# Performance work log

Hardware: AMD Instinct MI355X
Metric: run time of the kernel (lower is better)

Reference implementation:

```python
import jax, jax.numpy as jnp
import numpy as np


def setup_inputs() -> dict:
    key = jax.random.key(0)
    k1, k2 = jax.random.split(key)
    feature = jax.random.normal(k1, (4, 256, 60, 60), dtype=jnp.float32)
    mask_q = jax.random.uniform(k2, (4, 2, 60, 60), dtype=jnp.float32)
    return {"feature": feature, "mask_q": mask_q, "kernel": 1}


FG_THRES = 0.5
BG_THRES = 0.8
TOPK_FALLBACK = 12


def _sel_mask(p, thres):
    # boolean selection mask; falls back to top-12 pixels if nothing passes threshold
    m = p > thres
    topk_idx = jax.lax.top_k(p, TOPK_FALLBACK)[1]
    topk_m = jnp.zeros(p.shape, bool).at[topk_idx].set(True)
    return jnp.where(m.sum() > 0, m, topk_m)


def _ssp_single(feat, pred):
    # feat: [C, N], pred: [2, N] (ch0 = bg, ch1 = fg)
    pred_bg, pred_fg = pred[0], pred[1]
    fg_m = _sel_mask(pred_fg, FG_THRES)
    bg_m = _sel_mask(pred_bg, BG_THRES)

    def proto(m):
        mf = m.astype(feat.dtype)
        return (feat * mf[None, :]).sum(-1) / mf.sum()  # mean over selected cols

    fg_proto = proto(fg_m)  # [C]
    bg_proto = proto(bg_m)  # [C]

    # column-normalized features; selected-column sub-matmul == full matmul with
    # column-masked softmax (masked logits -> zero weight), identical math
    featn = feat / jnp.linalg.norm(feat, axis=0, keepdims=True)
    sim = (featn.T @ featn) * 2.0  # [N, N]
    logits = jnp.where(bg_m[None, :], sim, jnp.finfo(sim.dtype).min)
    w = jax.nn.softmax(logits, axis=-1)  # weights zero outside bg selection
    bg_local = (w @ feat.T).T  # [C, N]; == bg_sim @ bg_feat.T in torch code
    return fg_proto, bg_proto, bg_local


def reference(feature, mask_q, kernel):
    # kernel=True path of SSP_MatchingNet.forward: returns (FP_1, BP_1)
    bs, C, fh, fw = feature.shape
    feat_flat = feature.reshape(bs, C, fh * fw)
    pred = mask_q.reshape(bs, 2, -1)
    fg_p, bg_p, bg_loc = jax.vmap(_ssp_single)(feat_flat, pred)
    FP_1 = fg_p[:, :, None, None] * 1.0  # SSFP_1
    BP_1 = bg_p[:, :, None, None] * 0.3 + bg_loc.reshape(bs, C, fh, fw) * 0.7
    return FP_1, BP_1
```

## Files before the change

kernel.cpp:

```cpp
#include <hip/hip_runtime.h>
#include <math.h>
#include <float.h>

#define NPix 3600
#define NC   256
#define NB   4
#define MCAP 768

typedef __attribute__((ext_vector_type(8))) _Float16 half8v;
typedef __attribute__((ext_vector_type(4))) float float4v;

__device__ __forceinline__ unsigned short f2h(float x) {
  _Float16 h = (_Float16)x;
  unsigned short u; __builtin_memcpy(&u, &h, 2); return u;
}
__device__ __forceinline__ float h2f(unsigned short u) {
  _Float16 h; __builtin_memcpy(&h, &u, 2); return (float)h;
}

__device__ __forceinline__ void gld_lds16(const void* g, void* l) {
  __builtin_amdgcn_global_load_lds(
      (const __attribute__((address_space(1))) unsigned int*)g,
      (__attribute__((address_space(3))) unsigned int*)l, 16, 0, 0);
}

__global__ __launch_bounds__(256) void k_colnorm(const float* __restrict__ feature,
                                                 float* __restrict__ colnorm) {
  int b = blockIdx.y;
  int n = blockIdx.x * 256 + threadIdx.x;
  if (n >= NPix) return;
  const float* feat = feature + (size_t)b * NC * NPix;
  float acc = 0.f;
#pragma unroll 8
  for (int c = 0; c < NC; ++c) {
    float v = feat[(size_t)c * NPix + n];
    acc += v * v;
  }
  colnorm[b * NPix + n] = sqrtf(acc);
}

__device__ void block_top12(const float* __restrict__ p, int t,
                            float* s_rv, int* s_ri, int* s_chosen) {
  for (int k = 0; k < 12; ++k) {
    float best = -FLT_MAX;
    int bi = 0x7fffffff;
    for (int n = t; n < NPix; n += 1024) {
      bool excl = false;
      for (int j = 0; j < k; ++j)
        if (s_chosen[j] == n) excl = true;
      if (!excl) {
        float v = p[n];
        if (v > best || (v == best && n < bi)) { best = v; bi = n; }
      }
    }
    s_rv[t] = best; s_ri[t] = bi;
    __syncthreads();
    for (int d = 512; d > 0; d >>= 1) {
      if (t < d) {
        if (s_rv[t + d] > s_rv[t] ||
            (s_rv[t + d] == s_rv[t] && s_ri[t + d] < s_ri[t])) {
          s_rv[t] = s_rv[t + d]; s_ri[t] = s_ri[t + d];
        }
      }
      __syncthreads();
    }
    if (t == 0) s_chosen[k] = s_ri[0];
    __syncthreads();
  }
  if (t == 0) {
    for (int a = 1; a < 12; ++a) {
      int key = s_chosen[a]; int j = a - 1;
      while (j >= 0 && s_chosen[j] > key) { s_chosen[j + 1] = s_chosen[j]; --j; }
      s_chosen[j + 1] = key;
    }
  }
  __syncthreads();
}

__global__ __launch_bounds__(1024) void k_mask(const float* __restrict__ mask_q,
                                               unsigned char* __restrict__ fgm,
                                               unsigned char* __restrict__ bgm,
                                               int* __restrict__ bgsel,
                                               int* __restrict__ cnts) {
  int b = blockIdx.x;
  int t = threadIdx.x;
  int wv = t >> 6, l = t & 63;
  const float* pred_bg = mask_q + (size_t)b * 2 * NPix;
  const float* pred_fg = pred_bg + NPix;

  __shared__ int   s_wtot[16];
  __shared__ int   s_base[2];
  __shared__ float s_rv[1024];
  __shared__ int   s_ri[1024];
  __shared__ int   s_chosen[12];

  if (t == 0) { s_base[0] = 0; s_base[1] = 0; }
  __syncthreads();

  unsigned long long lmask = (1ull << l) - 1ull;

  for (int chunk = 0; chunk < NPix; chunk += 1024) {
    int n = chunk + t;
    int fgf = 0, bgf = 0;
    if (n < NPix) {
      fgf = pred_fg[n] > 0.5f ? 1 : 0;
      bgf = pred_bg[n] > 0.8f ? 1 : 0;
      fgm[b * NPix + n] = (unsigned char)fgf;
      bgm[b * NPix + n] = (unsigned char)bgf;
    }
    unsigned long long fb = __ballot(fgf != 0);
    unsigned long long bb = __ballot(bgf != 0);
    if (l == 0) s_wtot[wv] = __popcll(fb) | (__popcll(bb) << 16);
    __syncthreads();
    int fsum = 0, bsum = 0, bpre = 0;
#pragma unroll
    for (int w = 0; w < 16; ++w) {
      int v = s_wtot[w];
      if (w < wv) bpre += (v >> 16);
      fsum += v & 0xffff; bsum += (v >> 16);
    }
    if (bgf) {
      int pos = s_base[1] + bpre + (int)__popcll(bb & lmask);
      bgsel[b * NPix + pos] = n;
    }
    __syncthreads();
    if (t == 0) { s_base[0] += fsum; s_base[1] += bsum; }
    __syncthreads();
  }
  int fgcnt = s_base[0];
  int bgcnt = s_base[1];

  if (fgcnt == 0) {
    block_top12(pred_fg, t, s_rv, s_ri, s_chosen);
    if (t < 12) fgm[b * NPix + s_chosen[t]] = 1;
    fgcnt = 12;
    __syncthreads();
  }
  if (bgcnt == 0) {
    block_top12(pred_bg, t, s_rv, s_ri, s_chosen);
    if (t < 12) {
      bgm[b * NPix + s_chosen[t]] = 1;
      bgsel[b * NPix + t] = s_chosen[t];
    }
    bgcnt = 12;
    __syncthreads();
  }
  if (t == 0) { cnts[b] = fgcnt; cnts[4 + b] = bgcnt; }
}

__global__ __launch_bounds__(256) void k_proto(const float* __restrict__ feature,
                                               const unsigned char* __restrict__ fgm,
                                               const unsigned char* __restrict__ bgm,
                                               const int* __restrict__ cnts,
                                               float* __restrict__ out,
                                               float* __restrict__ bgproto) {
  int c = blockIdx.x, b = blockIdx.y, t = threadIdx.x;
  const float* frow = feature + ((size_t)b * NC + c) * NPix;
  float fs = 0.f, bs = 0.f;
  for (int n = t; n < NPix; n += 256) {
    float v = frow[n];
    fs += v * (float)fgm[b * NPix + n];
    bs += v * (float)bgm[b * NPix + n];
  }
  __shared__ float s1[256], s2[256];
  s1[t] = fs; s2[t] = bs;
  __syncthreads();
  for (int d = 128; d > 0; d >>= 1) {
    if (t < d) { s1[t] += s1[t + d]; s2[t] += s2[t + d]; }
    __syncthreads();
  }
  if (t == 0) {
    out[b * NC + c]     = s1[0] / (float)cnts[b];
    bgproto[b * NC + c] = s2[0] / (float)cnts[4 + b];
  }
}

__global__ __launch_bounds__(256) void k_normpack(const float* __restrict__ feature,
                                                  const unsigned char* __restrict__ fgm,
                                                  const unsigned char* __restrict__ bgm,
                                                  float* __restrict__ colnorm,
                                                  unsigned short* __restrict__ Qf,
                                                  float* __restrict__ pp) {
  int b = blockIdx.y, nt = blockIdx.x, t = threadIdx.x;
  int n0 = nt * 64;
  __shared__ float s_sq[16][68];
  __shared__ float s_inv[64];
  __shared__ float s_fg[64], s_bg[64];
  __shared__ unsigned int tl[64][65];
  __shared__ float traw[64][65];
  __shared__ float s_red[2][4][64];
  const float* fb = feature + (size_t)b * NC * NPix;

  int p4 = t & 15, cq = t >> 4;
  float sq0 = 0.f, sq1 = 0.f, sq2 = 0.f, sq3 = 0.f;
  if (n0 + 64 <= NPix) {
#pragma unroll
    for (int j = 0; j < 16; ++j) {
      const float* src = fb + (size_t)(cq * 16 + j) * NPix + n0 + p4 * 4;
      float4 v = *(const float4*)src;
      sq0 += v.x * v.x; sq1 += v.y * v.y; sq2 += v.z * v.z; sq3 += v.w * v.w;
    }
  } else {
#pragma unroll
    for (int j = 0; j < 16; ++j) {
      size_t base = (size_t)(cq * 16 + j) * NPix;
      int n = n0 + p4 * 4;
      float v0 = (n + 0 < NPix) ? fb[base + n + 0] : 0.f;
      float v1 = (n + 1 < NPix) ? fb[base + n + 1] : 0.f;
      float v2 = (n + 2 < NPix) ? fb[base + n + 2] : 0.f;
      float v3 = (n + 3 < NPix) ? fb[base + n + 3] : 0.f;
      sq0 += v0 * v0; sq1 += v1 * v1; sq2 += v2 * v2; sq3 += v3 * v3;
    }
  }
  s_sq[cq][p4 * 4 + 0] = sq0;
  s_sq[cq][p4 * 4 + 1] = sq1;
  s_sq[cq][p4 * 4 + 2] = sq2;
  s_sq[cq][p4 * 4 + 3] = sq3;
  __syncthreads();
  if (t < 64) {
    float acc = 0.f;
#pragma unroll
    for (int q = 0; q < 16; ++q) acc += s_sq[q][t];
    float nrm = sqrtf(acc);
    int n = n0 + t;
    s_inv[t] = (n < NPix) ? 1.f / nrm : 0.f;
    if (n < NPix) colnorm[b * NPix + n] = nrm;
    s_fg[t] = (n < NPix) ? (float)fgm[b * NPix + n] : 0.f;
    s_bg[t] = (n < NPix) ? (float)bgm[b * NPix + n] : 0.f;
  }
  __syncthreads();

  unsigned short* QfB = Qf + (size_t)b * NPix * NC;
  int nl = t & 63;
  int nn = n0 + nl;
  bool inr = nn < NPix;
  float invn = s_inv[nl];
  for (int cs = 0; cs < 4; ++cs) {
    int c0 = cs * 64;
#pragma unroll
    for (int i = 0; i < 16; ++i) {
      int cl = (t >> 6) + 4 * i;
      float raw = inr ? fb[(size_t)(c0 + cl) * NPix + nn] : 0.f;
      traw[cl][nl] = raw;
      tl[cl][nl] = (unsigned int)f2h(raw * invn);
    }
    __syncthreads();
#pragma unroll
    for (int i = 0; i < 8; ++i) {
      int idx = t + 256 * i;
      int n = idx >> 5;
      int cp = idx & 31;
      int row = n0 + n;
      if (row < NPix) {
        unsigned int u = (tl[2 * cp][n] & 0xffffu) | (tl[2 * cp + 1][n] << 16);
        *(unsigned int*)&QfB[(size_t)row * NC + c0 + 2 * cp] = u;
      }
    }
    {
      int cl = t & 63, pq = t >> 6;
      float pf = 0.f, pb = 0.f;
#pragma unroll
      for (int k = 0; k < 16; ++k) {
        int p = pq * 16 + k;
        float feat = traw[cl][p];
        pf += feat * s_fg[p];
        pb += feat * s_bg[p];
      }
      s_red[0][pq][cl] = pf;
      s_red[1][pq][cl] = pb;
    }
    __syncthreads();
    if (t < 128) {
      int m = t >> 6, cl = t & 63;
      float s = s_red[m][0][cl] + s_red[m][1][cl] + s_red[m][2][cl] + s_red[m][3][cl];
      pp[((size_t)(b * 57 + nt) * 2 + m) * 256 + c0 + cl] = s;
    }
    __syncthreads();
  }
}

__global__ __launch_bounds__(256) void k_vg(const unsigned short* __restrict__ Qf,
                                            const float* __restrict__ colnorm,
                                            const int* __restrict__ cnts,
                                            const int* __restrict__ bgsel,
                                            unsigned short* __restrict__ Vg,
                                            const float* __restrict__ pp,
                                            float* __restrict__ out,
                                            float* __restrict__ bgproto,
                                            unsigned short* __restrict__ wbuf,
                                            float* __restrict__ wpart) {
  int b = blockIdx.z;
  int x = blockIdx.x;
  int t = threadIdx.x;

  __shared__ __align__(16) char smem[32768];

  if (x == 222) {
    int c = t;
    float f = 0.f, g = 0.f;
    for (int nt = 0; nt < 57; ++nt) {
      const float* base = pp + (size_t)(b * 57 + nt) * 2 * 256;
      f += base[c];
      g += base[256 + c];
    }
    out[b * NC + c]     = f / (float)cnts[b];
    bgproto[b * NC + c] = g / (float)cnts[4 + b];
    return;
  }

  int M = cnts[4 + b];
  if (M > MCAP) return;

  if (x >= 174) {
    int u = x - 174;
    int jt = u >> 2, cs = u & 3;
    int j0 = jt * 64, c0 = cs * 64;
    unsigned short* tl = (unsigned short*)smem;
    const size_t qoff = (size_t)b * NPix * NC;
#pragma unroll
    for (int i = 0; i < 16; ++i) {
      int idx = t + 256 * i; int j = idx >> 6, ch = idx & 63;
      int jg = j0 + j;
      float v = 0.f;
      if (jg < M) {
        int src = bgsel[b * NPix + jg];
        v = h2f(Qf[qoff + (size_t)src * NC + c0 + ch]) * colnorm[b * NPix + src];
      }
      tl[j * 73 + ch] = f2h(v);
    }
    __syncthreads();
#pragma unroll
    for (int i = 0; i < 16; ++i) {
      int idx = t + 256 * i; int ch = idx >> 6, j = idx & 63;
      Vg[((size_t)b * NC + c0 + ch) * MCAP + j0 + j] = tl[j * 73 + ch];
    }
    return;
  }

  int rt = x % 29, jt = x / 29;
  if (jt * 128 >= M) return;
  int wv = t >> 6, l = t & 63;
  int n0 = rt * 128, j0 = jt * 128;

  unsigned short* Ah = (unsigned short*)smem;
  unsigned short* Bh = (unsigned short*)(smem + 32768 / 2);

  const unsigned short* QfB = Qf + (size_t)b * NPix * NC;

  size_t asrc[4];
  int    aslt[4];
#pragma unroll
  for (int i = 0; i < 4; ++i) {
    int u = i * 256 + wv * 64 + l;
    int r = u >> 3, sl = u & 7;
    int grow = n0 + r; if (grow > NPix - 1) grow = NPix - 1;
    asrc[i] = (size_t)grow * NC;
    aslt[i] = (sl ^ (r & 7)) << 3;
  }
  size_t bsrc[4];
  int    bslt[4];
#pragma unroll
  for (int i = 0; i < 4; ++i) {
    int u = i * 256 + wv * 64 + l;
    int r = u >> 3, sl = u & 7;
    int jg = j0 + r;
    int src = (jg < M) ? bgsel[b * NPix + jg] : 0;
    bsrc[i] = (size_t)src * NC;
    bslt[i] = (sl ^ (r & 7)) << 3;
  }

  int lr = l & 15;
  int lk = l >> 4;

  float4v acc[2][8];
#pragma unroll
  for (int rf = 0; rf < 2; ++rf)
#pragma unroll
    for (int cf = 0; cf < 8; ++cf) { float4v z = {0.f,0.f,0.f,0.f}; acc[rf][cf] = z; }

  for (int cc = 0; cc < 4; ++cc) {
    int cbase = cc * 64;
#pragma unroll
    for (int i = 0; i < 4; ++i) {
      int ldso = (i * 256 + wv * 64) * 16;
      gld_lds16(QfB + asrc[i] + cbase + aslt[i], (char*)Ah + ldso);
    }
#pragma unroll
    for (int i = 0; i < 4; ++i) {
      int ldso = (i * 256 + wv * 64) * 16;
      gld_lds16(QfB + bsrc[i] + cbase + bslt[i], (char*)Bh + ldso);
    }
    __syncthreads();

#pragma unroll
    for (int kk = 0; kk < 2; ++kk) {
      int kslot = kk * 4 + lk;
      half8v ah[2];
#pragma unroll
      for (int rf = 0; rf < 2; ++rf) {
        int r = wv * 32 + rf * 16 + lr;
        int s = (kslot ^ (r & 7)) << 3;
        ah[rf] = *(const half8v*)&Ah[r * 64 + s];
      }
#pragma unroll
      for (int cf = 0; cf < 8; ++cf) {
        int j = cf * 16 + lr;
        int s = (kslot ^ (j & 7)) << 3;
        half8v bh = *(const half8v*)&Bh[j * 64 + s];
#pragma unroll
        for (int rf = 0; rf < 2; ++rf)
          acc[rf][cf] = __builtin_amdgcn_mfma_f32_16x16x32_f16(ah[rf], bh, acc[rf][cf], 0, 0, 0);
      }
    }
    __syncthreads();
  }

  float rs[2][4];
#pragma unroll
  for (int rf = 0; rf < 2; ++rf)
#pragma unroll
    for (int i = 0; i < 4; ++i) rs[rf][i] = 0.f;

#pragma unroll
  for (int rf = 0; rf < 2; ++rf)
#pragma unroll
    for (int cf = 0; cf < 8; ++cf)
#pragma unroll
      for (int i = 0; i < 4; ++i) {
        int row = n0 + wv * 32 + rf * 16 + lk * 4 + i;
        int j = j0 + cf * 16 + lr;
        float s = acc[rf][cf][i];
        unsigned short w16 = (j < M) ? f2h(__expf(2.f * s - 2.f)) : (unsigned short)0;
        if (row < NPix)
          wbuf[((size_t)b * NPix + row) * MCAP + j] = w16;
        rs[rf][i] += h2f(w16);
      }

#pragma unroll
  for (int rf = 0; rf < 2; ++rf)
#pragma unroll
    for (int i = 0; i < 4; ++i) {
      float v = rs[rf][i];
      v += __shfl_xor(v, 1);
      v += __shfl_xor(v, 2);
      v += __shfl_xor(v, 4);
      v += __shfl_xor(v, 8);
      int row = n0 + wv * 32 + rf * 16 + lk * 4 + i;
      if (lr == 0 && row < NPix)
        wpart[((size_t)b * NPix + row) * 12 + jt] = v;
    }
}

__global__ __launch_bounds__(256, 3) void k_gemm2e(const unsigned short* __restrict__ wbuf,
                                                   const unsigned short* __restrict__ Vg,
                                                   const int* __restrict__ cnts,
                                                   const float* __restrict__ wpart,
                                                   const float* __restrict__ bgproto,
                                                   float* __restrict__ out) {
  int b = blockIdx.z; int M = cnts[4 + b]; if (M > MCAP) return;
  int rt = blockIdx.x, cs = blockIdx.y;
  int t = threadIdx.x, wv = t >> 6, l = t & 63;
  int n0 = rt * 128, c0 = cs * 128;
  int arow0 = n0 + wv * 32 + (l & 15);
  int arow1 = arow0 + 16;
  if (arow0 > NPix - 1) arow0 = NPix - 1;
  if (arow1 > NPix - 1) arow1 = NPix - 1;
  const unsigned short* wr0 = wbuf + ((size_t)b * NPix + arow0) * MCAP + (l >> 4) * 8;
  const unsigned short* wr1 = wbuf + ((size_t)b * NPix + arow1) * MCAP + (l >> 4) * 8;
  const unsigned short* vb  = Vg + ((size_t)b * NC + c0 + (l & 15)) * MCAP + (l >> 4) * 8;

  __shared__ float trans[64][129];
  __shared__ float s_linv[128];
  __shared__ float s_bp[128];

  float4v acc[2][8];
#pragma unroll
  for (int rf = 0; rf < 2; ++rf)
#pragma unroll
    for (int cf = 0; cf < 8; ++cf) { float4v z = {0.f,0.f,0.f,0.f}; acc[rf][cf] = z; }

  int nkk = (M + 31) >> 5;
  for (int kk = 0; kk < nkk; ++kk) {
    half8v a0 = *(const half8v*)(wr0 + kk * 32);
    half8v a1 = *(const half8v*)(wr1 + kk * 32);
#pragma unroll
    for (int cf = 0; cf < 8; ++cf) {
      half8v bv = *(const half8v*)(vb + (size_t)cf * 16 * MCAP + kk * 32);
      acc[0][cf] = __builtin_amdgcn_mfma_f32_16x16x32_f16(a0, bv, acc[0][cf], 0, 0, 0);
      acc[1][cf] = __builtin_amdgcn_mfma_f32_16x16x32_f16(a1, bv, acc[1][cf], 0, 0, 0);
    }
  }

  if (t < 128) {
    int row = n0 + t;
    if (row < NPix) {
      const float* wp = wpart + ((size_t)b * NPix + row) * 12;
      int njt = (M + 127) >> 7;
      float s = 0.f;
      for (int j = 0; j < njt; ++j) s += wp[j];
      s_linv[t] = 1.f / s;
    } else s_linv[t] = 0.f;
    s_bp[t] = bgproto[b * NC + c0 + t];
  }

  int g = l >> 4;
  float* outBP = out + NB * NC;
#pragma unroll
  for (int half = 0; half < 2; ++half) {
    __syncthreads();
#pragma unroll
    for (int cfl = 0; cfl < 4; ++cfl) {
      int cf = half * 4 + cfl;
#pragma unroll
      for (int rf = 0; rf < 2; ++rf)
#pragma unroll
        for (int i = 0; i < 4; ++i) {
          int c_l = cfl * 16 + (l & 15);
          int n_l = wv * 32 + rf * 16 + g * 4 + i;
          trans[c_l][n_l] = acc[rf][cf][i];
        }
    }
    __syncthreads();
#pragma unroll
    for (int it = 0; it < 8; ++it) {
      int idx = t + 256 * it;
      int c_l = idx >> 5;
      int q   = idx & 31;
      int n   = n0 + q * 4;
      if (n < NPix) {
        float bpv = s_bp[half * 64 + c_l];
        float4 o;
        o.x = bpv * 0.3f + trans[c_l][q * 4 + 0] * s_linv[q * 4 + 0] * 0.7f;
        o.y = bpv * 0.3f + trans[c_l][q * 4 + 1] * s_linv[q * 4 + 1] * 0.7f;
        o.z = bpv * 0.3f + trans[c_l][q * 4 + 2] * s_linv[q * 4 + 2] * 0.7f;
        o.w = bpv * 0.3f + trans[c_l][q * 4 + 3] * s_linv[q * 4 + 3] * 0.7f;
        *(float4*)&outBP[((size_t)b * NC + c0 + half * 64 + c_l) * NPix + n] = o;
      }
    }
  }
}

__global__ __launch_bounds__(256) void k_attn(const float* __restrict__ feature,
                                              const float* __restrict__ colnorm,
                                              const int* __restrict__ cnts,
                                              const int* __restrict__ bgsel,
                                              const float* __restrict__ bgproto,
                                              float* __restrict__ out,
                                              int gate) {
  int b = blockIdx.y;
  int M = cnts[4 + b];
  if (gate && M <= MCAP) return;
  int tile = blockIdx.x;
  int t = threadIdx.x;
  int rl  = t >> 4;
  int l16 = t & 15;
  int row = tile * 16 + rl;
  const float* feat = feature + (size_t)b * NC * NPix;

  __shared__ float s_k[32][NC];
  __shared__ float s_vn[32];

  float inv_n = 1.f / colnorm[b * NPix + row];
  float q[16];
#pragma unroll
  for (int k = 0; k < 4; ++k)
#pragma unroll
    for (int i = 0; i < 4; ++i) {
      int c = l16 * 4 + 64 * k + i;
      q[k * 4 + i] = feat[(size_t)c * NPix + row] * inv_n;
    }

  float l_acc = 0.f;
  float O[16];
#pragma unroll
  for (int i = 0; i < 16; ++i) O[i] = 0.f;

  for (int kt = 0; kt < M; kt += 32) {
    int jmax = min(32, M - kt);
    __syncthreads();
    for (int u = t; u < 32 * 64; u += 256) {
      int jj = u >> 6;
      int cc = (u & 63) << 2;
      if (jj < jmax) {
        int src = bgsel[b * NPix + kt + jj];
        float inv = 1.f / colnorm[b * NPix + src];
        float4 v;
        v.x = feat[(size_t)(cc + 0) * NPix + src] * inv;
        v.y = feat[(size_t)(cc + 1) * NPix + src] * inv;
        v.z = feat[(size_t)(cc + 2) * NPix + src] * inv;
        v.w = feat[(size_t)(cc + 3) * NPix + src] * inv;
        *(float4*)&s_k[jj][cc] = v;
      }
    }
    if (t < 32)
      s_vn[t] = (t < jmax) ? colnorm[b * NPix + bgsel[b * NPix + kt + t]] : 0.f;
    __syncthreads();

    for (int j = 0; j < jmax; ++j) {
      float kv[16];
      float s = 0.f;
#pragma unroll
      for (int k = 0; k < 4; ++k) {
        float4 v4 = *(const float4*)&s_k[j][l16 * 4 + 64 * k];
        kv[k * 4 + 0] = v4.x; kv[k * 4 + 1] = v4.y;
        kv[k * 4 + 2] = v4.z; kv[k * 4 + 3] = v4.w;
        s += q[k * 4 + 0] * v4.x + q[k * 4 + 1] * v4.y +
             q[k * 4 + 2] * v4.z + q[k * 4 + 3] * v4.w;
      }
      s += __shfl_xor(s, 1);
      s += __shfl_xor(s, 2);
      s += __shfl_xor(s, 4);
      s += __shfl_xor(s, 8);
      float e = __expf(2.f * s - 2.f);
      l_acc += e;
      float ev = e * s_vn[j];
#pragma unroll
      for (int i = 0; i < 16; ++i) O[i] += ev * kv[i];
    }
  }

  float inv_l = 1.f / l_acc;
  float* outBP = out + NB * NC;
  const float* bp = bgproto + b * NC;
#pragma unroll
  for (int k = 0; k < 4; ++k)
#pragma unroll
    for (int i = 0; i < 4; ++i) {
      int c = l16 * 4 + 64 * k + i;
      outBP[((size_t)b * NC + c) * NPix + row] =
          bp[c] * 0.3f + O[k * 4 + i] * inv_l * 0.7f;
    }
}

extern "C" void kernel_launch(void* const* d_in, const int* in_sizes, int n_in,
                              void* d_out, int out_size, void* d_ws, size_t ws_size,
                              hipStream_t stream) {
  const float* feature = (const float*)d_in[0];
  const float* mask_q  = (const float*)d_in[1];
  float* out = (float*)d_out;
  char* ws = (char*)d_ws;

  const size_t BIG_NEED = 32428160ULL;
  if (ws_size >= BIG_NEED) {
    float* colnorm   = (float*)(ws + 0);
    float* bgproto   = (float*)(ws + 115200);
    int*   cnts      = (int*)  (ws + 119296);
    int*   bgsel     = (int*)  (ws + 119552);
    unsigned char* fgm = (unsigned char*)(ws + 177152);
    unsigned char* bgm = (unsigned char*)(ws + 191552);
    float* pp        = (float*)(ws + 205952);
    unsigned short* Vg  = (unsigned short*)(ws + 672896);
    unsigned short* Qf  = (unsigned short*)(ws + 2245760);
    unsigned short* wbuf = (unsigned short*)(ws + 9618560);
    float* wpart     = (float*)(ws + 31736960);

    k_mask    <<<NB,               1024, 0, stream>>>(mask_q, fgm, bgm, bgsel, cnts);
    k_normpack<<<dim3(57, NB),     256, 0, stream>>>(feature, fgm, bgm, colnorm, Qf, pp);
    k_vg      <<<dim3(223, 1, NB), 256, 0, stream>>>(Qf, colnorm, cnts, bgsel, Vg,
                                                     pp, out, bgproto, wbuf, wpart);
    k_gemm2e  <<<dim3(29, 2, NB),  256, 0, stream>>>(wbuf, Vg, cnts, wpart, bgproto, out);
    k_attn    <<<dim3(225, NB),    256, 0, stream>>>(feature, colnorm, cnts, bgsel,
                                                     bgproto, out, 1);
  } else {
    float* colnorm  = (float*)(ws + 0);
    float* bgproto  = (float*)(ws + 115200);
    int*   cnts     = (int*)  (ws + 119296);
    int*   bgsel    = (int*)  (ws + 119552);
    unsigned char* fgm = (unsigned char*)(ws + 177152);
    unsigned char* bgm = (unsigned char*)(ws + 191552);

    k_colnorm<<<dim3(15, NB), 256, 0, stream>>>(feature, colnorm);
    k_mask   <<<NB,           1024, 0, stream>>>(mask_q, fgm, bgm, bgsel, cnts);
    k_proto  <<<dim3(NC, NB), 256, 0, stream>>>(feature, fgm, bgm, cnts, out, bgproto);
    k_attn   <<<dim3(225, NB),256, 0, stream>>>(feature, colnorm, cnts, bgsel,
                                                bgproto, out, 0);
  }
}
```

Baseline: 91.00 us.

## Fuse fallback attention into gemm2e launch and reuse register-held features in normpack

The fallback attention path (for batches with more than MCAP selected background pixels) moves into extra blocks of the k_gemm2e launch, which removes a separate k_attn launch that mostly exited early. k_normpack now keeps the float4 feature values from its norm pass in registers and writes them into the shared transpose tiles, instead of loading the feature tensor from global memory a second time. The cost is more registers per thread in normpack (16 float4) and a larger fused kernel whose shared-memory use is the maximum of both paths. This may lower occupancy.

```diff
diff --git a/kernel.cpp b/kernel.cpp
--- a/kernel.cpp
+++ b/kernel.cpp
@@ -192,12 +192,13 @@
   const float* fb = feature + (size_t)b * NC * NPix;
 
   int p4 = t & 15, cq = t >> 4;
+  float4 raw[16];
   float sq0 = 0.f, sq1 = 0.f, sq2 = 0.f, sq3 = 0.f;
   if (n0 + 64 <= NPix) {
 #pragma unroll
     for (int j = 0; j < 16; ++j) {
-      const float* src = fb + (size_t)(cq * 16 + j) * NPix + n0 + p4 * 4;
-      float4 v = *(const float4*)src;
+      float4 v = *(const float4*)(fb + (size_t)(cq * 16 + j) * NPix + n0 + p4 * 4);
+      raw[j] = v;
       sq0 += v.x * v.x; sq1 += v.y * v.y; sq2 += v.z * v.z; sq3 += v.w * v.w;
     }
   } else {
@@ -205,11 +206,13 @@
     for (int j = 0; j < 16; ++j) {
       size_t base = (size_t)(cq * 16 + j) * NPix;
       int n = n0 + p4 * 4;
-      float v0 = (n + 0 < NPix) ? fb[base + n + 0] : 0.f;
-      float v1 = (n + 1 < NPix) ? fb[base + n + 1] : 0.f;
-      float v2 = (n + 2 < NPix) ? fb[base + n + 2] : 0.f;
-      float v3 = (n + 3 < NPix) ? fb[base + n + 3] : 0.f;
-      sq0 += v0 * v0; sq1 += v1 * v1; sq2 += v2 * v2; sq3 += v3 * v3;
+      float4 v;
+      v.x = (n + 0 < NPix) ? fb[base + n + 0] : 0.f;
+      v.y = (n + 1 < NPix) ? fb[base + n + 1] : 0.f;
+      v.z = (n + 2 < NPix) ? fb[base + n + 2] : 0.f;
+      v.w = (n + 3 < NPix) ? fb[base + n + 3] : 0.f;
+      raw[j] = v;
+      sq0 += v.x * v.x; sq1 += v.y * v.y; sq2 += v.z * v.z; sq3 += v.w * v.w;
     }
   }
   s_sq[cq][p4 * 4 + 0] = sq0;
@@ -231,18 +234,22 @@
   __syncthreads();
 
   unsigned short* QfB = Qf + (size_t)b * NPix * NC;
-  int nl = t & 63;
-  int nn = n0 + nl;
-  bool inr = nn < NPix;
-  float invn = s_inv[nl];
+  int clbase = (cq & 3) * 16;
+  int nlb = p4 * 4;
+  float inv0 = s_inv[nlb + 0], inv1 = s_inv[nlb + 1];
+  float inv2 = s_inv[nlb + 2], inv3 = s_inv[nlb + 3];
   for (int cs = 0; cs < 4; ++cs) {
     int c0 = cs * 64;
-#pragma unroll
-    for (int i = 0; i < 16; ++i) {
-      int cl = (t >> 6) + 4 * i;
-      float raw = inr ? fb[(size_t)(c0 + cl) * NPix + nn] : 0.f;
-      traw[cl][nl] = raw;
-      tl[cl][nl] = (unsigned int)f2h(raw * invn);
+    if ((cq >> 2) == cs) {
+#pragma unroll
+      for (int j = 0; j < 16; ++j) {
+        int cl = clbase + j;
+        float4 v = raw[j];
+        traw[cl][nlb + 0] = v.x;  tl[cl][nlb + 0] = (unsigned int)f2h(v.x * inv0);
+        traw[cl][nlb + 1] = v.y;  tl[cl][nlb + 1] = (unsigned int)f2h(v.y * inv1);
+        traw[cl][nlb + 2] = v.z;  tl[cl][nlb + 2] = (unsigned int)f2h(v.z * inv2);
+        traw[cl][nlb + 3] = v.w;  tl[cl][nlb + 3] = (unsigned int)f2h(v.w * inv3);
+      }
     }
     __syncthreads();
 #pragma unroll
@@ -343,7 +350,7 @@
   int n0 = rt * 128, j0 = jt * 128;
 
   unsigned short* Ah = (unsigned short*)smem;
-  unsigned short* Bh = (unsigned short*)(smem + 32768 / 2);
+  unsigned short* Bh = (unsigned short*)(smem + 16384);
 
   const unsigned short* QfB = Qf + (size_t)b * NPix * NC;
 
@@ -456,10 +463,102 @@
                                                    const int* __restrict__ cnts,
                                                    const float* __restrict__ wpart,
                                                    const float* __restrict__ bgproto,
+                                                   const float* __restrict__ feature,
+                                                   const float* __restrict__ colnorm,
+                                                   const int* __restrict__ bgsel,
                                                    float* __restrict__ out) {
-  int b = blockIdx.z; int M = cnts[4 + b]; if (M > MCAP) return;
-  int rt = blockIdx.x, cs = blockIdx.y;
-  int t = threadIdx.x, wv = t >> 6, l = t & 63;
+  int b = blockIdx.z; int M = cnts[4 + b];
+  int x = blockIdx.x;
+  int t = threadIdx.x;
+
+  __shared__ __align__(16) char smem[34816];
+
+  if (x >= 58) {
+    if (M <= MCAP) return;
+    int tile = x - 58;
+    int rl  = t >> 4;
+    int l16 = t & 15;
+    int row = tile * 16 + rl;
+    const float* feat = feature + (size_t)b * NC * NPix;
+    float* s_k  = (float*)smem;
+    float* s_vn = (float*)(smem + 32768);
+
+    float inv_n = 1.f / colnorm[b * NPix + row];
+    float q[16];
+#pragma unroll
+    for (int k = 0; k < 4; ++k)
+#pragma unroll
+      for (int i = 0; i < 4; ++i) {
+        int c = l16 * 4 + 64 * k + i;
+        q[k * 4 + i] = feat[(size_t)c * NPix + row] * inv_n;
+      }
+
+    float l_acc = 0.f;
+    float O[16];
+#pragma unroll
+    for (int i = 0; i < 16; ++i) O[i] = 0.f;
+
+    for (int kt = 0; kt < M; kt += 32) {
+      int jmax = min(32, M - kt);
+      __syncthreads();
+      for (int u = t; u < 32 * 64; u += 256) {
+        int jj = u >> 6;
+        int cc = (u & 63) << 2;
+        if (jj < jmax) {
+          int src = bgsel[b * NPix + kt + jj];
+          float inv = 1.f / colnorm[b * NPix + src];
+          float4 v;
+          v.x = feat[(size_t)(cc + 0) * NPix + src] * inv;
+          v.y = feat[(size_t)(cc + 1) * NPix + src] * inv;
+          v.z = feat[(size_t)(cc + 2) * NPix + src] * inv;
+          v.w = feat[(size_t)(cc + 3) * NPix + src] * inv;
+          *(float4*)&s_k[jj * 256 + cc] = v;
+        }
+      }
+      if (t < 32)
+        s_vn[t] = (t < jmax) ? colnorm[b * NPix + bgsel[b * NPix + kt + t]] : 0.f;
+      __syncthreads();
+
+      for (int j = 0; j < jmax; ++j) {
+        float kv[16];
+        float s = 0.f;
+#pragma unroll
+        for (int k = 0; k < 4; ++k) {
+          float4 v4 = *(const float4*)&s_k[j * 256 + l16 * 4 + 64 * k];
+          kv[k * 4 + 0] = v4.x; kv[k * 4 + 1] = v4.y;
+          kv[k * 4 + 2] = v4.z; kv[k * 4 + 3] = v4.w;
+          s += q[k * 4 + 0] * v4.x + q[k * 4 + 1] * v4.y +
+               q[k * 4 + 2] * v4.z + q[k * 4 + 3] * v4.w;
+        }
+        s += __shfl_xor(s, 1);
+        s += __shfl_xor(s, 2);
+        s += __shfl_xor(s, 4);
+        s += __shfl_xor(s, 8);
+        float e = __expf(2.f * s - 2.f);
+        l_acc += e;
+        float ev = e * s_vn[j];
+#pragma unroll
+        for (int i = 0; i < 16; ++i) O[i] += ev * kv[i];
+      }
+    }
+
+    float inv_l = 1.f / l_acc;
+    float* outBP = out + NB * NC;
+    const float* bp = bgproto + b * NC;
+#pragma unroll
+    for (int k = 0; k < 4; ++k)
+#pragma unroll
+      for (int i = 0; i < 4; ++i) {
+        int c = l16 * 4 + 64 * k + i;
+        outBP[((size_t)b * NC + c) * NPix + row] =
+            bp[c] * 0.3f + O[k * 4 + i] * inv_l * 0.7f;
+      }
+    return;
+  }
+
+  if (M > MCAP) return;
+  int rt = x % 29, cs = x / 29;
+  int wv = t >> 6, l = t & 63;
   int n0 = rt * 128, c0 = cs * 128;
   int arow0 = n0 + wv * 32 + (l & 15);
   int arow1 = arow0 + 16;
@@ -469,9 +568,9 @@
   const unsigned short* wr1 = wbuf + ((size_t)b * NPix + arow1) * MCAP + (l >> 4) * 8;
   const unsigned short* vb  = Vg + ((size_t)b * NC + c0 + (l & 15)) * MCAP + (l >> 4) * 8;
 
-  __shared__ float trans[64][129];
-  __shared__ float s_linv[128];
-  __shared__ float s_bp[128];
+  float* trans  = (float*)smem;
+  float* s_linv = (float*)(smem + 33024);
+  float* s_bp   = (float*)(smem + 33536);
 
   float4v acc[2][8];
 #pragma unroll
@@ -517,7 +616,7 @@
         for (int i = 0; i < 4; ++i) {
           int c_l = cfl * 16 + (l & 15);
           int n_l = wv * 32 + rf * 16 + g * 4 + i;
-          trans[c_l][n_l] = acc[rf][cf][i];
+          trans[c_l * 129 + n_l] = acc[rf][cf][i];
         }
     }
     __syncthreads();
@@ -530,10 +629,10 @@
       if (n < NPix) {
         float bpv = s_bp[half * 64 + c_l];
         float4 o;
-        o.x = bpv * 0.3f + trans[c_l][q * 4 + 0] * s_linv[q * 4 + 0] * 0.7f;
-        o.y = bpv * 0.3f + trans[c_l][q * 4 + 1] * s_linv[q * 4 + 1] * 0.7f;
-        o.z = bpv * 0.3f + trans[c_l][q * 4 + 2] * s_linv[q * 4 + 2] * 0.7f;
-        o.w = bpv * 0.3f + trans[c_l][q * 4 + 3] * s_linv[q * 4 + 3] * 0.7f;
+        o.x = bpv * 0.3f + trans[c_l * 129 + q * 4 + 0] * s_linv[q * 4 + 0] * 0.7f;
+        o.y = bpv * 0.3f + trans[c_l * 129 + q * 4 + 1] * s_linv[q * 4 + 1] * 0.7f;
+        o.z = bpv * 0.3f + trans[c_l * 129 + q * 4 + 2] * s_linv[q * 4 + 2] * 0.7f;
+        o.w = bpv * 0.3f + trans[c_l * 129 + q * 4 + 3] * s_linv[q * 4 + 3] * 0.7f;
         *(float4*)&outBP[((size_t)b * NC + c0 + half * 64 + c_l) * NPix + n] = o;
       }
     }
@@ -545,11 +644,9 @@
                                               const int* __restrict__ cnts,
                                               const int* __restrict__ bgsel,
                                               const float* __restrict__ bgproto,
-                                              float* __restrict__ out,
-                                              int gate) {
+                                              float* __restrict__ out) {
   int b = blockIdx.y;
   int M = cnts[4 + b];
-  if (gate && M <= MCAP) return;
   int tile = blockIdx.x;
   int t = threadIdx.x;
   int rl  = t >> 4;
@@ -658,9 +755,8 @@
     k_normpack<<<dim3(57, NB),     256, 0, stream>>>(feature, fgm, bgm, colnorm, Qf, pp);
     k_vg      <<<dim3(223, 1, NB), 256, 0, stream>>>(Qf, colnorm, cnts, bgsel, Vg,
                                                      pp, out, bgproto, wbuf, wpart);
-    k_gemm2e  <<<dim3(29, 2, NB),  256, 0, stream>>>(wbuf, Vg, cnts, wpart, bgproto, out);
-    k_attn    <<<dim3(225, NB),    256, 0, stream>>>(feature, colnorm, cnts, bgsel,
-                                                     bgproto, out, 1);
+    k_gemm2e  <<<dim3(283, 1, NB), 256, 0, stream>>>(wbuf, Vg, cnts, wpart, bgproto,
+                                                     feature, colnorm, bgsel, out);
   } else {
     float* colnorm  = (float*)(ws + 0);
     float* bgproto  = (float*)(ws + 115200);
@@ -673,6 +769,6 @@
     k_mask   <<<NB,           1024, 0, stream>>>(mask_q, fgm, bgm, bgsel, cnts);
     k_proto  <<<dim3(NC, NB), 256, 0, stream>>>(feature, fgm, bgm, cnts, out, bgproto);
     k_attn   <<<dim3(225, NB),256, 0, stream>>>(feature, colnorm, cnts, bgsel,
-                                                bgproto, out, 0);
-  }
-}
+                                                bgproto, out);
+  }
+}
```

After: 127.0 us. 39.6% more time.
